# Optimization experiments

Measured on AMD Instinct MI355X. Metric: run time of the kernel, lower is better.

## Reference

```python
import jax, jax.numpy as jnp
import numpy as np

B, IN_DIM, OUT_DIM = 4096, 8192, 8192

# Each of the 16 gates op_i(a,b) is affine in (1, a, b, a*b).
# Rows: [const, coef_a, coef_b, coef_ab] for gate i = 0..15.
GATE_COEF = np.array([
    [0.,  0.,  0.,  0.],   # 0: zeros
    [0.,  0.,  0.,  1.],   # 1: a*b
    [0.,  1.,  0., -1.],   # 2: a - a*b
    [0.,  1.,  0.,  0.],   # 3: a
    [0.,  0.,  1., -1.],   # 4: b - a*b
    [0.,  0.,  1.,  0.],   # 5: b
    [0.,  1.,  1., -2.],   # 6: a + b - 2ab (xor)
    [0.,  1.,  1., -1.],   # 7: a + b - ab (or)
    [1., -1., -1.,  1.],   # 8: 1 - (a + b - ab)
    [1., -1., -1.,  2.],   # 9: 1 - (a + b - 2ab)
    [1.,  0., -1.,  0.],   # 10: 1 - b
    [1.,  0., -1.,  1.],   # 11: 1 - b + ab
    [1., -1.,  0.,  0.],   # 12: 1 - a
    [1., -1.,  0.,  1.],   # 13: 1 - a + ab
    [1.,  0.,  0., -1.],   # 14: 1 - ab
    [1.,  0.,  0.,  0.],   # 15: ones
], dtype=np.float32)


def setup_inputs() -> dict:
    key = jax.random.key(0)
    k1, k2, k3, k4 = jax.random.split(key, 4)
    x = jax.random.uniform(k1, (B, IN_DIM), dtype=jnp.float32)
    weights = jax.random.normal(k2, (OUT_DIM, 16), dtype=jnp.float32)
    idx0 = jax.random.randint(k3, (OUT_DIM,), 0, IN_DIM)
    idx1 = jax.random.randint(k4, (OUT_DIM,), 0, IN_DIM)
    return {"x": x, "weights": weights, "idx0": idx0, "idx1": idx1}


def reference(x, weights, idx0, idx1):
    # training path: soft mixture over 16 gates
    p = jax.nn.softmax(weights, axis=-1)          # [out_dim, 16]
    c = p @ jnp.asarray(GATE_COEF)                # [out_dim, 4]: sum_i p_i * op_i collapsed
    a = x[:, idx0]                                # [B, out_dim]
    b = x[:, idx1]                                # [B, out_dim]
    return c[:, 0] + c[:, 1] * a + c[:, 2] * b + c[:, 3] * (a * b)
```

## Files before the change

kernel.cpp:

```cpp
#include <hip/hip_runtime.h>

#define IN_DIM 8192
#define OUT_DIM 8192
#define NROWS 4096
#define THREADS 512
#define RPB 2
#define JITERS (OUT_DIM / (THREADS * 4))

typedef float v4f __attribute__((ext_vector_type(4)));

__device__ __constant__ float GATE_COEF[16][4] = {
    {0.f, 0.f, 0.f, 0.f}, {0.f, 0.f, 0.f, 1.f}, {0.f, 1.f, 0.f, -1.f}, {0.f, 1.f, 0.f, 0.f},
    {0.f, 0.f, 1.f, -1.f}, {0.f, 0.f, 1.f, 0.f}, {0.f, 1.f, 1.f, -2.f}, {0.f, 1.f, 1.f, -1.f},
    {1.f, -1.f, -1.f, 1.f}, {1.f, -1.f, -1.f, 2.f}, {1.f, 0.f, -1.f, 0.f}, {1.f, 0.f, -1.f, 1.f},
    {1.f, -1.f, 0.f, 0.f}, {1.f, -1.f, 0.f, 1.f}, {1.f, 0.f, 0.f, -1.f}, {1.f, 0.f, 0.f, 0.f}};

__global__ __launch_bounds__(256) void compute_c_kernel(const float* __restrict__ w,
                                                        float* __restrict__ cp) {
    int j = blockIdx.x * blockDim.x + threadIdx.x;
    if (j >= OUT_DIM) return;
    const float4* wv = (const float4*)(w + (size_t)j * 16);
    float4 w0 = wv[0], w1 = wv[1], w2 = wv[2], w3 = wv[3];
    float wa[16] = {w0.x, w0.y, w0.z, w0.w, w1.x, w1.y, w1.z, w1.w,
                    w2.x, w2.y, w2.z, w2.w, w3.x, w3.y, w3.z, w3.w};
    float m = wa[0];
#pragma unroll
    for (int k = 1; k < 16; ++k) m = fmaxf(m, wa[k]);
    float p[16];
    float s = 0.f;
#pragma unroll
    for (int k = 0; k < 16; ++k) {
        p[k] = __expf(wa[k] - m);
        s += p[k];
    }
    float inv = 1.f / s;
    float c0 = 0.f, c1 = 0.f, c2 = 0.f, c3 = 0.f;
#pragma unroll
    for (int k = 0; k < 16; ++k) {
        c0 = fmaf(p[k], GATE_COEF[k][0], c0);
        c1 = fmaf(p[k], GATE_COEF[k][1], c1);
        c2 = fmaf(p[k], GATE_COEF[k][2], c2);
        c3 = fmaf(p[k], GATE_COEF[k][3], c3);
    }
    cp[j] = c0 * inv;
    cp[j + OUT_DIM] = c1 * inv;
    cp[j + 2 * OUT_DIM] = c2 * inv;
    cp[j + 3 * OUT_DIM] = c3 * inv;
}

__global__ __launch_bounds__(THREADS, 4) void gate_kernel(const float* __restrict__ x,
                                                          const float* __restrict__ cp,
                                                          const int* __restrict__ idx0,
                                                          const int* __restrict__ idx1,
                                                          float* __restrict__ out) {
    __shared__ float rows[RPB * IN_DIM];
    const int r0 = blockIdx.x * RPB;
    const int tid = threadIdx.x;

    const v4f* xr0 = (const v4f*)(x + (size_t)r0 * IN_DIM);
    const v4f* xr1 = (const v4f*)(x + (size_t)(r0 + 1) * IN_DIM);
    v4f* rv0 = (v4f*)rows;
    v4f* rv1 = (v4f*)(rows + IN_DIM);
    v4f st[8];
#pragma unroll
    for (int t = 0; t < 4; ++t) st[t] = __builtin_nontemporal_load(xr0 + tid + t * THREADS);
#pragma unroll
    for (int t = 0; t < 4; ++t) st[4 + t] = __builtin_nontemporal_load(xr1 + tid + t * THREADS);

    const int j0 = tid * 4;
    int4 pi0 = *(const int4*)(idx0 + j0);
    int4 pi1 = *(const int4*)(idx1 + j0);

#pragma unroll
    for (int t = 0; t < 4; ++t) rv0[tid + t * THREADS] = st[t];
#pragma unroll
    for (int t = 0; t < 4; ++t) rv1[tid + t * THREADS] = st[4 + t];
    __syncthreads();

    const float* __restrict__ c0p = cp;
    const float* __restrict__ c1p = cp + OUT_DIM;
    const float* __restrict__ c2p = cp + 2 * OUT_DIM;
    const float* __restrict__ c3p = cp + 3 * OUT_DIM;
    float* o0 = out + (size_t)r0 * OUT_DIM;
    float* o1 = out + (size_t)(r0 + 1) * OUT_DIM;

#pragma unroll
    for (int k = 0; k < JITERS; ++k) {
        const int j = k * (THREADS * 4) + tid * 4;
        const int4 i0 = pi0;
        const int4 i1 = pi1;
        if (k < JITERS - 1) {
            const int jn = j + THREADS * 4;
            pi0 = *(const int4*)(idx0 + jn);
            pi1 = *(const int4*)(idx1 + jn);
        }
        const v4f c0v = *(const v4f*)(c0p + j);
        const v4f c1v = *(const v4f*)(c1p + j);
        const v4f c2v = *(const v4f*)(c2p + j);
        const v4f c3v = *(const v4f*)(c3p + j);
        v4f a0, b0, a1, b1;
        a0.x = rows[i0.x]; a0.y = rows[i0.y]; a0.z = rows[i0.z]; a0.w = rows[i0.w];
        b0.x = rows[i1.x]; b0.y = rows[i1.y]; b0.z = rows[i1.z]; b0.w = rows[i1.w];
        a1.x = rows[IN_DIM + i0.x]; a1.y = rows[IN_DIM + i0.y];
        a1.z = rows[IN_DIM + i0.z]; a1.w = rows[IN_DIM + i0.w];
        b1.x = rows[IN_DIM + i1.x]; b1.y = rows[IN_DIM + i1.y];
        b1.z = rows[IN_DIM + i1.z]; b1.w = rows[IN_DIM + i1.w];

        const v4f r0v = c0v + c1v * a0 + c2v * b0 + c3v * (a0 * b0);
        const v4f r1v = c0v + c1v * a1 + c2v * b1 + c3v * (a1 * b1);
        __builtin_nontemporal_store(r0v, (v4f*)(o0 + j));
        __builtin_nontemporal_store(r1v, (v4f*)(o1 + j));
    }
}

extern "C" void kernel_launch(void* const* d_in, const int* in_sizes, int n_in,
                              void* d_out, int out_size, void* d_ws, size_t ws_size,
                              hipStream_t stream) {
    const float* x = (const float*)d_in[0];
    const float* weights = (const float*)d_in[1];
    const int* idx0 = (const int*)d_in[2];
    const int* idx1 = (const int*)d_in[3];
    float* out = (float*)d_out;
    float* cp = (float*)d_ws;

    compute_c_kernel<<<OUT_DIM / 256, 256, 0, stream>>>(weights, cp);
    gate_kernel<<<NROWS / RPB, THREADS, 0, stream>>>(x, cp, idx0, idx1, out);
}
```

Baseline: 233.7 us.

## Fuse softmax coefficients into persistent gate kernel with double-buffered row staging

Removes the separate coefficient kernel and instead computes the softmax-collapsed gate coefficients per thread in registers, keeping indices and coefficients resident for the whole block. The gate kernel becomes persistent: 256 blocks of 1024 threads, each walking 16 rows, with a two-slot LDS buffer and a register prefetch of the next row so the global load overlaps the gather and compute of the current row. This drops the launch and the repeated coefficient and index reloads, but it raises register pressure, leaves only 256 blocks to cover the GPU, and puts a barrier on every row.

```diff
diff --git a/kernel.cpp b/kernel.cpp
--- a/kernel.cpp
+++ b/kernel.cpp
@@ -3,126 +3,120 @@
 #define IN_DIM 8192
 #define OUT_DIM 8192
 #define NROWS 4096
-#define THREADS 512
-#define RPB 2
-#define JITERS (OUT_DIM / (THREADS * 4))
+#define THREADS 1024
+#define GRID 256
+#define RPB (NROWS / GRID)
+#define JG (OUT_DIM / (THREADS * 4))
+
+static_assert(GRID * RPB == NROWS, "row partition");
+static_assert(JG * THREADS * 4 == OUT_DIM, "col partition");
 
 typedef float v4f __attribute__((ext_vector_type(4)));
 
-__device__ __constant__ float GATE_COEF[16][4] = {
-    {0.f, 0.f, 0.f, 0.f}, {0.f, 0.f, 0.f, 1.f}, {0.f, 1.f, 0.f, -1.f}, {0.f, 1.f, 0.f, 0.f},
-    {0.f, 0.f, 1.f, -1.f}, {0.f, 0.f, 1.f, 0.f}, {0.f, 1.f, 1.f, -2.f}, {0.f, 1.f, 1.f, -1.f},
-    {1.f, -1.f, -1.f, 1.f}, {1.f, -1.f, -1.f, 2.f}, {1.f, 0.f, -1.f, 0.f}, {1.f, 0.f, -1.f, 1.f},
-    {1.f, -1.f, 0.f, 0.f}, {1.f, -1.f, 0.f, 1.f}, {1.f, 0.f, 0.f, -1.f}, {1.f, 0.f, 0.f, 0.f}};
+#define BLOCK_SYNC_LDS()                                   \
+  do {                                                     \
+    asm volatile("s_waitcnt lgkmcnt(0)" ::: "memory");     \
+    __builtin_amdgcn_s_barrier();                          \
+    asm volatile("" ::: "memory");                         \
+  } while (0)
 
-__global__ __launch_bounds__(256) void compute_c_kernel(const float* __restrict__ w,
-                                                        float* __restrict__ cp) {
-    int j = blockIdx.x * blockDim.x + threadIdx.x;
-    if (j >= OUT_DIM) return;
-    const float4* wv = (const float4*)(w + (size_t)j * 16);
-    float4 w0 = wv[0], w1 = wv[1], w2 = wv[2], w3 = wv[3];
+static __device__ __forceinline__ void softmax_c(const float* __restrict__ w, int jbase,
+                                                 v4f* C0, v4f* C1, v4f* C2, v4f* C3) {
+  static constexpr float G[16][4] = {
+      {0.f, 0.f, 0.f, 0.f}, {0.f, 0.f, 0.f, 1.f}, {0.f, 1.f, 0.f, -1.f}, {0.f, 1.f, 0.f, 0.f},
+      {0.f, 0.f, 1.f, -1.f}, {0.f, 0.f, 1.f, 0.f}, {0.f, 1.f, 1.f, -2.f}, {0.f, 1.f, 1.f, -1.f},
+      {1.f, -1.f, -1.f, 1.f}, {1.f, -1.f, -1.f, 2.f}, {1.f, 0.f, -1.f, 0.f}, {1.f, 0.f, -1.f, 1.f},
+      {1.f, -1.f, 0.f, 0.f}, {1.f, -1.f, 0.f, 1.f}, {1.f, 0.f, 0.f, -1.f}, {1.f, 0.f, 0.f, 0.f}};
+#pragma unroll
+  for (int q = 0; q < 4; ++q) {
+    const float4* wp = (const float4*)(w + (size_t)(jbase + q) * 16);
+    float4 w0 = wp[0], w1 = wp[1], w2 = wp[2], w3 = wp[3];
     float wa[16] = {w0.x, w0.y, w0.z, w0.w, w1.x, w1.y, w1.z, w1.w,
                     w2.x, w2.y, w2.z, w2.w, w3.x, w3.y, w3.z, w3.w};
     float m = wa[0];
 #pragma unroll
     for (int k = 1; k < 16; ++k) m = fmaxf(m, wa[k]);
+    float s = 0.f;
     float p[16];
-    float s = 0.f;
+#pragma unroll
+    for (int k = 0; k < 16; ++k) { p[k] = __expf(wa[k] - m); s += p[k]; }
+    const float inv = 1.f / s;
+    float a0 = 0.f, a1 = 0.f, a2 = 0.f, a3 = 0.f;
 #pragma unroll
     for (int k = 0; k < 16; ++k) {
-        p[k] = __expf(wa[k] - m);
-        s += p[k];
+      a0 = fmaf(p[k], G[k][0], a0);
+      a1 = fmaf(p[k], G[k][1], a1);
+      a2 = fmaf(p[k], G[k][2], a2);
+      a3 = fmaf(p[k], G[k][3], a3);
     }
-    float inv = 1.f / s;
-    float c0 = 0.f, c1 = 0.f, c2 = 0.f, c3 = 0.f;
-#pragma unroll
-    for (int k = 0; k < 16; ++k) {
-        c0 = fmaf(p[k], GATE_COEF[k][0], c0);
-        c1 = fmaf(p[k], GATE_COEF[k][1], c1);
-        c2 = fmaf(p[k], GATE_COEF[k][2], c2);
-        c3 = fmaf(p[k], GATE_COEF[k][3], c3);
-    }
-    cp[j] = c0 * inv;
-    cp[j + OUT_DIM] = c1 * inv;
-    cp[j + 2 * OUT_DIM] = c2 * inv;
-    cp[j + 3 * OUT_DIM] = c3 * inv;
+    (*C0)[q] = a0 * inv; (*C1)[q] = a1 * inv; (*C2)[q] = a2 * inv; (*C3)[q] = a3 * inv;
+  }
 }
 
-__global__ __launch_bounds__(THREADS, 4) void gate_kernel(const float* __restrict__ x,
-                                                          const float* __restrict__ cp,
-                                                          const int* __restrict__ idx0,
-                                                          const int* __restrict__ idx1,
-                                                          float* __restrict__ out) {
-    __shared__ float rows[RPB * IN_DIM];
-    const int r0 = blockIdx.x * RPB;
-    const int tid = threadIdx.x;
+__global__ __launch_bounds__(THREADS, 4) void gate_fused(
+    const float* __restrict__ x, const float* __restrict__ w,
+    const int* __restrict__ idx0, const int* __restrict__ idx1,
+    float* __restrict__ out) {
+  __shared__ __align__(16) float buf[2][IN_DIM];
+  const int tid = threadIdx.x;
+  const int r0 = blockIdx.x * RPB;
 
-    const v4f* xr0 = (const v4f*)(x + (size_t)r0 * IN_DIM);
-    const v4f* xr1 = (const v4f*)(x + (size_t)(r0 + 1) * IN_DIM);
-    v4f* rv0 = (v4f*)rows;
-    v4f* rv1 = (v4f*)(rows + IN_DIM);
-    v4f st[8];
+  int4 i0[JG], i1[JG];
+  v4f C0[JG], C1[JG], C2[JG], C3[JG];
 #pragma unroll
-    for (int t = 0; t < 4; ++t) st[t] = __builtin_nontemporal_load(xr0 + tid + t * THREADS);
+  for (int g = 0; g < JG; ++g) {
+    const int j = tid * 4 + g * (THREADS * 4);
+    i0[g] = *(const int4*)(idx0 + j);
+    i1[g] = *(const int4*)(idx1 + j);
+    softmax_c(w, j, &C0[g], &C1[g], &C2[g], &C3[g]);
+  }
+
+  v4f ra[2];
+  const float* x0 = x + (size_t)r0 * IN_DIM;
 #pragma unroll
-    for (int t = 0; t < 4; ++t) st[4 + t] = __builtin_nontemporal_load(xr1 + tid + t * THREADS);
+  for (int t = 0; t < 2; ++t) ra[t] = __builtin_nontemporal_load((const v4f*)x0 + tid + t * THREADS);
+#pragma unroll
+  for (int t = 0; t < 2; ++t) ((v4f*)buf[0])[tid + t * THREADS] = ra[t];
+#pragma unroll
+  for (int t = 0; t < 2; ++t)
+    ra[t] = __builtin_nontemporal_load((const v4f*)(x0 + IN_DIM) + tid + t * THREADS);
+  BLOCK_SYNC_LDS();
 
-    const int j0 = tid * 4;
-    int4 pi0 = *(const int4*)(idx0 + j0);
-    int4 pi1 = *(const int4*)(idx1 + j0);
-
+#pragma unroll 1
+  for (int p = 0; p < RPB; ++p) {
+    if (p + 1 < RPB) {
+      v4f* dst = (v4f*)buf[(p + 1) & 1];
 #pragma unroll
-    for (int t = 0; t < 4; ++t) rv0[tid + t * THREADS] = st[t];
+      for (int t = 0; t < 2; ++t) dst[tid + t * THREADS] = ra[t];
+    }
+    if (p + 2 < RPB) {
+      const float* xs = x + (size_t)(r0 + p + 2) * IN_DIM;
 #pragma unroll
-    for (int t = 0; t < 4; ++t) rv1[tid + t * THREADS] = st[4 + t];
-    __syncthreads();
-
-    const float* __restrict__ c0p = cp;
-    const float* __restrict__ c1p = cp + OUT_DIM;
-    const float* __restrict__ c2p = cp + 2 * OUT_DIM;
-    const float* __restrict__ c3p = cp + 3 * OUT_DIM;
-    float* o0 = out + (size_t)r0 * OUT_DIM;
-    float* o1 = out + (size_t)(r0 + 1) * OUT_DIM;
-
+      for (int t = 0; t < 2; ++t)
+        ra[t] = __builtin_nontemporal_load((const v4f*)xs + tid + t * THREADS);
+    }
+    const float* bufc = buf[p & 1];
+    float* o = out + (size_t)(r0 + p) * OUT_DIM;
 #pragma unroll
-    for (int k = 0; k < JITERS; ++k) {
-        const int j = k * (THREADS * 4) + tid * 4;
-        const int4 i0 = pi0;
-        const int4 i1 = pi1;
-        if (k < JITERS - 1) {
-            const int jn = j + THREADS * 4;
-            pi0 = *(const int4*)(idx0 + jn);
-            pi1 = *(const int4*)(idx1 + jn);
-        }
-        const v4f c0v = *(const v4f*)(c0p + j);
-        const v4f c1v = *(const v4f*)(c1p + j);
-        const v4f c2v = *(const v4f*)(c2p + j);
-        const v4f c3v = *(const v4f*)(c3p + j);
-        v4f a0, b0, a1, b1;
-        a0.x = rows[i0.x]; a0.y = rows[i0.y]; a0.z = rows[i0.z]; a0.w = rows[i0.w];
-        b0.x = rows[i1.x]; b0.y = rows[i1.y]; b0.z = rows[i1.z]; b0.w = rows[i1.w];
-        a1.x = rows[IN_DIM + i0.x]; a1.y = rows[IN_DIM + i0.y];
-        a1.z = rows[IN_DIM + i0.z]; a1.w = rows[IN_DIM + i0.w];
-        b1.x = rows[IN_DIM + i1.x]; b1.y = rows[IN_DIM + i1.y];
-        b1.z = rows[IN_DIM + i1.z]; b1.w = rows[IN_DIM + i1.w];
-
-        const v4f r0v = c0v + c1v * a0 + c2v * b0 + c3v * (a0 * b0);
-        const v4f r1v = c0v + c1v * a1 + c2v * b1 + c3v * (a1 * b1);
-        __builtin_nontemporal_store(r0v, (v4f*)(o0 + j));
-        __builtin_nontemporal_store(r1v, (v4f*)(o1 + j));
+    for (int g = 0; g < JG; ++g) {
+      const int4 ia = i0[g], ib = i1[g];
+      v4f a, b;
+      a.x = bufc[ia.x]; a.y = bufc[ia.y]; a.z = bufc[ia.z]; a.w = bufc[ia.w];
+      b.x = bufc[ib.x]; b.y = bufc[ib.y]; b.z = bufc[ib.z]; b.w = bufc[ib.w];
+      const v4f r = C0[g] + C1[g] * a + C2[g] * b + C3[g] * (a * b);
+      __builtin_nontemporal_store(r, (v4f*)(o + tid * 4 + g * (THREADS * 4)));
     }
+    BLOCK_SYNC_LDS();
+  }
 }
 
 extern "C" void kernel_launch(void* const* d_in, const int* in_sizes, int n_in,
                               void* d_out, int out_size, void* d_ws, size_t ws_size,
                               hipStream_t stream) {
-    const float* x = (const float*)d_in[0];
-    const float* weights = (const float*)d_in[1];
-    const int* idx0 = (const int*)d_in[2];
-    const int* idx1 = (const int*)d_in[3];
-    float* out = (float*)d_out;
-    float* cp = (float*)d_ws;
-
-    compute_c_kernel<<<OUT_DIM / 256, 256, 0, stream>>>(weights, cp);
-    gate_kernel<<<NROWS / RPB, THREADS, 0, stream>>>(x, cp, idx0, idx1, out);
+  const float* x = (const float*)d_in[0];
+  const float* weights = (const float*)d_in[1];
+  const int* idx0 = (const int*)d_in[2];
+  const int* idx1 = (const int*)d_in[3];
+  float* out = (float*)d_out;
+  gate_fused<<<GRID, THREADS, 0, stream>>>(x, weights, idx0, idx1, out);
 }
```

After: 246.6 us. 5.5% more time.
